# Kernel tuning notes

Hardware: AMD Instinct MI355X
Metric: run time of the kernel (lower is better)

## Reference

```python
import jax, jax.numpy as jnp
import numpy as np

N_NODES = 50000
N_EDGES = 800000
IN_FEAT = 512
HEADS = 4
OUT_FEAT = 64


def setup_inputs() -> dict:
    key = jax.random.key(0)
    k1, k2, k3 = jax.random.split(key, 3)
    x = jax.random.normal(k1, (N_NODES, IN_FEAT), dtype=jnp.float32)
    # W corresponds to nn.Linear(in, heads*out, bias=False).weight: (H*F, in)
    W = jax.random.normal(k2, (HEADS * OUT_FEAT, IN_FEAT), dtype=jnp.float32) * (1.0 / np.sqrt(IN_FEAT))
    edge_index = jax.random.randint(k3, (2, N_EDGES), 0, N_NODES, dtype=jnp.int32)
    return {"x": x, "W": W, "edge_index": edge_index}


def reference(x, W, edge_index):
    # h = W(x) viewed as (N, H, F)
    n = x.shape[0]
    hf = W.shape[0]
    h = (x @ W.T).reshape(n, HEADS, hf // HEADS)
    src, dst = edge_index[0], edge_index[1]
    # scatter-mean of h[src] into dst buckets (single O(E) pass, replaces per-node loop)
    msg = h[src]                                             # (E, H, F)
    summed = jax.ops.segment_sum(msg, dst, num_segments=n)   # (N, H, F)
    cnt = jax.ops.segment_sum(jnp.ones((edge_index.shape[1],), h.dtype), dst, num_segments=n)
    mean = summed / jnp.maximum(cnt, 1.0)[:, None, None]
    # nodes with no in-edges keep their own transformed features
    out = jnp.where((cnt > 0)[:, None, None], mean, h)
    return out.reshape(n, hf)
```

## Files before the change

kernel.cpp:

```cpp
#include <hip/hip_runtime.h>
#include <hip/hip_bf16.h>

#define N_NODES 50000
#define N_EDGES 800000
#define IN_FEAT 512
#define HF 256
#define BM 128
#define BN 256
#define BK 32
#define CAP 64
#define GEMM_BLOCKS 391
#define FILL_BLOCKS 218

typedef short short8 __attribute__((ext_vector_type(8)));
typedef float f32x4 __attribute__((ext_vector_type(4)));

__device__ __forceinline__ unsigned short f2bf(float f) {
    union { float f; unsigned u; } c{f};
    unsigned r = c.u + 0x7FFFu + ((c.u >> 16) & 1u);
    return (unsigned short)(r >> 16);
}
__device__ __forceinline__ float bf2f(unsigned short b) {
    union { unsigned u; float f; } c;
    c.u = ((unsigned)b) << 16;
    return c.f;
}
__device__ __forceinline__ short8 pack8(const float4& a, const float4& b) {
    short8 v;
    v[0] = (short)f2bf(a.x); v[1] = (short)f2bf(a.y);
    v[2] = (short)f2bf(a.z); v[3] = (short)f2bf(a.w);
    v[4] = (short)f2bf(b.x); v[5] = (short)f2bf(b.y);
    v[6] = (short)f2bf(b.z); v[7] = (short)f2bf(b.w);
    return v;
}
__device__ __forceinline__ void gload16(const void* g, void* l) {
    __builtin_amdgcn_global_load_lds(
        (const __attribute__((address_space(1))) unsigned int*)g,
        (__attribute__((address_space(3))) unsigned int*)l, 16, 0, 0);
}

__global__ __launch_bounds__(64) void convw_kernel(const float* __restrict__ Wm,
                                                   unsigned short* __restrict__ Wb) {
    const int row = blockIdx.x;
    const int t = threadIdx.x;
    const int slice = t >> 2;
    const int p = t & 3;
    const int lc = p ^ ((row >> 1) & 3);
    const float* g = Wm + (size_t)row * IN_FEAT + slice * 32 + lc * 8;
    const float4 v0 = *(const float4*)(g);
    const float4 v1 = *(const float4*)(g + 4);
    *(short8*)(Wb + (size_t)row * IN_FEAT + slice * 32 + p * 8) = pack8(v0, v1);
}

__global__ __launch_bounds__(512) void gemm_fill_kernel(const float* __restrict__ X,
                                                        const unsigned short* __restrict__ Wb,
                                                        unsigned short* __restrict__ H,
                                                        const int* __restrict__ ei,
                                                        int* __restrict__ cnt,
                                                        int* __restrict__ bucket) {
    if (blockIdx.x >= GEMM_BLOCKS) {
        const int cb = blockIdx.x - GEMM_BLOCKS;
        const int stride = FILL_BLOCKS * 512;
        for (int e = cb * 512 + threadIdx.x; e < N_EDGES; e += stride) {
            const int src = ei[e];
            const int dst = ei[N_EDGES + e];
            const int pos = atomicAdd(&cnt[dst], 1);
            if (pos < CAP) bucket[dst * CAP + pos] = src;
        }
        return;
    }

    __shared__ float Af[2][BM * BK];
    __shared__ unsigned short Bsh[2][BN * BK];

    const int t    = threadIdx.x;
    const int lane = t & 63;
    const int w    = t >> 6;
    const int wr   = w >> 2;
    const int wc   = w & 3;
    const int brow = blockIdx.x * BM;
    const int l15  = lane & 15;

    const int sa0 = w * 2, sa1 = w * 2 + 1;

    int aro0 = sa0 * 8 + (lane >> 3);
    int aro1 = sa1 * 8 + (lane >> 3);
    int ag0 = brow + aro0; if (ag0 >= N_NODES) ag0 = N_NODES - 1;
    int ag1 = brow + aro1; if (ag1 >= N_NODES) ag1 = N_NODES - 1;
    const int alc0 = ((lane & 7) ^ (aro0 & 7)) * 4;
    const int alc1 = ((lane & 7) ^ (aro1 & 7)) * 4;
    const float* asrc0 = X + (size_t)ag0 * IN_FEAT + alc0;
    const float* asrc1 = X + (size_t)ag1 * IN_FEAT + alc1;

    const int bro0 = sa0 * 16 + (lane >> 2);
    const int bro1 = sa1 * 16 + (lane >> 2);
    const unsigned short* bsrc0 = Wb + (size_t)bro0 * IN_FEAT + (lane & 3) * 8;
    const unsigned short* bsrc1 = Wb + (size_t)bro1 * IN_FEAT + (lane & 3) * 8;

    f32x4 acc[4][4] = {};

    gload16(asrc0, &Af[0][sa0 * 256]);
    gload16(asrc1, &Af[0][sa1 * 256]);
    gload16(bsrc0, &Bsh[0][sa0 * 512]);
    gload16(bsrc1, &Bsh[0][sa1 * 512]);
    __syncthreads();

    int cur = 0;
    for (int kt = 0; kt < IN_FEAT; kt += BK) {
        const int kn = kt + BK;
        if (kn < IN_FEAT) {
            const int nb = cur ^ 1;
            gload16(asrc0 + kn, &Af[nb][sa0 * 256]);
            gload16(asrc1 + kn, &Af[nb][sa1 * 256]);
            gload16(bsrc0 + kn, &Bsh[nb][sa0 * 512]);
            gload16(bsrc1 + kn, &Bsh[nb][sa1 * 512]);
        }

        const int c0 = (lane >> 4) * 2;
        const int cb0 = lane >> 4;
        short8 a[4], b[4];
#pragma unroll
        for (int n = 0; n < 4; ++n) {
            const int rt = wc * 64 + n * 16 + l15;
            b[n] = *(const short8*)(&Bsh[cur][rt * BK + ((cb0 ^ ((rt >> 1) & 3)) << 3)]);
        }
#pragma unroll
        for (int m = 0; m < 4; ++m) {
            const int rt = wr * 64 + m * 16 + l15;
            const float4 x0 = *(const float4*)(&Af[cur][rt * BK + ((c0 ^ (rt & 7)) << 2)]);
            const float4 x1 = *(const float4*)(&Af[cur][rt * BK + (((c0 + 1) ^ (rt & 7)) << 2)]);
            a[m] = pack8(x0, x1);
        }
#pragma unroll
        for (int m = 0; m < 4; ++m)
#pragma unroll
            for (int n = 0; n < 4; ++n)
                acc[m][n] = __builtin_amdgcn_mfma_f32_16x16x32_bf16(a[m], b[n], acc[m][n], 0, 0, 0);

        __syncthreads();
        cur ^= 1;
    }

#pragma unroll
    for (int m = 0; m < 4; ++m) {
        const int row0 = brow + wr * 64 + m * 16 + (lane >> 4) * 4;
#pragma unroll
        for (int n = 0; n < 4; ++n) {
            const int col = wc * 64 + n * 16 + l15;
#pragma unroll
            for (int j = 0; j < 4; ++j) {
                const int row = row0 + j;
                if (row < N_NODES) H[(size_t)row * HF + col] = f2bf(acc[m][n][j]);
            }
        }
    }
}

__global__ __launch_bounds__(256) void aggregate_kernel(const unsigned short* __restrict__ h,
                                                        const int* __restrict__ cnt,
                                                        const int* __restrict__ bucket,
                                                        float* __restrict__ out) {
    const int node = (int)(((size_t)blockIdx.x * blockDim.x + threadIdx.x) >> 6);
    const int lane = threadIdx.x & 63;
    if (node >= N_NODES) return;
    int c = cnt[node];
    if (c > CAP) c = CAP;
    const int base = node * CAP;

    float a0 = 0.f, a1 = 0.f, a2 = 0.f, a3 = 0.f;

    int i = 0;
    for (; i + 4 <= c; i += 4) {
        const int s0 = bucket[base + i + 0];
        const int s1 = bucket[base + i + 1];
        const int s2 = bucket[base + i + 2];
        const int s3 = bucket[base + i + 3];
        const ushort4 v0 = *(const ushort4*)(h + (size_t)s0 * HF + lane * 4);
        const ushort4 v1 = *(const ushort4*)(h + (size_t)s1 * HF + lane * 4);
        const ushort4 v2 = *(const ushort4*)(h + (size_t)s2 * HF + lane * 4);
        const ushort4 v3 = *(const ushort4*)(h + (size_t)s3 * HF + lane * 4);
        a0 += bf2f(v0.x) + bf2f(v1.x) + bf2f(v2.x) + bf2f(v3.x);
        a1 += bf2f(v0.y) + bf2f(v1.y) + bf2f(v2.y) + bf2f(v3.y);
        a2 += bf2f(v0.z) + bf2f(v1.z) + bf2f(v2.z) + bf2f(v3.z);
        a3 += bf2f(v0.w) + bf2f(v1.w) + bf2f(v2.w) + bf2f(v3.w);
    }
    for (; i < c; ++i) {
        const int s0 = bucket[base + i];
        const ushort4 v0 = *(const ushort4*)(h + (size_t)s0 * HF + lane * 4);
        a0 += bf2f(v0.x); a1 += bf2f(v0.y); a2 += bf2f(v0.z); a3 += bf2f(v0.w);
    }

    float4 r;
    if (c > 0) {
        const float inv = 1.0f / (float)c;
        r.x = a0 * inv; r.y = a1 * inv; r.z = a2 * inv; r.w = a3 * inv;
    } else {
        const ushort4 v = *(const ushort4*)(h + (size_t)node * HF + lane * 4);
        r.x = bf2f(v.x); r.y = bf2f(v.y); r.z = bf2f(v.z); r.w = bf2f(v.w);
    }
    *(float4*)(out + (size_t)node * HF + lane * 4) = r;
}

extern "C" void kernel_launch(void* const* d_in, const int* in_sizes, int n_in,
                              void* d_out, int out_size, void* d_ws, size_t ws_size,
                              hipStream_t stream) {
    const float* x = (const float*)d_in[0];
    const float* W = (const float*)d_in[1];
    const int* ei  = (const int*)d_in[2];
    float* out = (float*)d_out;

    char* ws = (char*)d_ws;
    unsigned short* h = (unsigned short*)ws;
    int* bucket = (int*)(ws + (size_t)N_NODES * HF * 2);
    int* cnt    = (int*)((char*)bucket + (size_t)N_NODES * CAP * 4);
    unsigned short* Wb = (unsigned short*)((char*)cnt + (size_t)(N_NODES + 64) * 4);

    hipMemsetAsync(cnt, 0, (size_t)N_NODES * sizeof(int), stream);

    convw_kernel<<<HF, 64, 0, stream>>>(W, Wb);

    gemm_fill_kernel<<<GEMM_BLOCKS + FILL_BLOCKS, 512, 0, stream>>>(x, Wb, h, ei, cnt, bucket);

    aggregate_kernel<<<(N_NODES * 64 + 255) / 256, 256, 0, stream>>>(h, cnt, bucket, out);
}
```

Before: 116.3 us.

## Triple-buffer A tiles, load B directly to registers, fuse counter zeroing

The GEMM now keeps the converted weight operand out of shared memory. Each wave loads its B fragments straight from global memory into registers, one K-step ahead. The X tile uses a three-stage LDS ring with explicit vmcnt waits and a single barrier per iteration instead of two syncthreads, and the final K-step is peeled out of the loop. The separate memset of the edge counters is folded into the weight-conversion kernel to save a launch. The weight swizzle is removed, and in exchange B traffic now goes through per-wave global loads that rely on L2 reuse across blocks.

After: 139.4 us. +19.8%, slower.

```diff
diff --git a/kernel.cpp b/kernel.cpp
--- a/kernel.cpp
+++ b/kernel.cpp
@@ -8,9 +8,12 @@
 #define BM 128
 #define BN 256
 #define BK 32
+#define NT 16
 #define CAP 64
 #define GEMM_BLOCKS 391
 #define FILL_BLOCKS 218
+#define CONV_BLOCKS 256
+#define ZERO_BLOCKS 200
 
 typedef short short8 __attribute__((ext_vector_type(8)));
 typedef float f32x4 __attribute__((ext_vector_type(4)));
@@ -39,17 +42,25 @@
         (__attribute__((address_space(3))) unsigned int*)l, 16, 0, 0);
 }
 
-__global__ __launch_bounds__(64) void convw_kernel(const float* __restrict__ Wm,
-                                                   unsigned short* __restrict__ Wb) {
-    const int row = blockIdx.x;
-    const int t = threadIdx.x;
-    const int slice = t >> 2;
-    const int p = t & 3;
-    const int lc = p ^ ((row >> 1) & 3);
-    const float* g = Wm + (size_t)row * IN_FEAT + slice * 32 + lc * 8;
-    const float4 v0 = *(const float4*)(g);
-    const float4 v1 = *(const float4*)(g + 4);
-    *(short8*)(Wb + (size_t)row * IN_FEAT + slice * 32 + p * 8) = pack8(v0, v1);
+__global__ __launch_bounds__(64) void convw_init_kernel(const float* __restrict__ Wm,
+                                                        unsigned short* __restrict__ Wb,
+                                                        int* __restrict__ cnt) {
+    if (blockIdx.x < CONV_BLOCKS) {
+        const int row = blockIdx.x;
+        const int t = threadIdx.x;
+        const float* g = Wm + (size_t)row * IN_FEAT + t * 8;
+        const float4 v0 = *(const float4*)(g);
+        const float4 v1 = *(const float4*)(g + 4);
+        *(short8*)(Wb + (size_t)row * IN_FEAT + t * 8) = pack8(v0, v1);
+    } else {
+        const int i = ((blockIdx.x - CONV_BLOCKS) * 64 + threadIdx.x) * 4;
+        if (i + 3 < N_NODES) {
+            int4 z = {0, 0, 0, 0};
+            *(int4*)(cnt + i) = z;
+        } else {
+            for (int k = 0; k < 4 && i + k < N_NODES; ++k) cnt[i + k] = 0;
+        }
+    }
 }
 
 __global__ __launch_bounds__(512) void gemm_fill_kernel(const float* __restrict__ X,
@@ -70,8 +81,7 @@
         return;
     }
 
-    __shared__ float Af[2][BM * BK];
-    __shared__ unsigned short Bsh[2][BN * BK];
+    __shared__ float Af[3][BM * BK];
 
     const int t    = threadIdx.x;
     const int lane = t & 63;
@@ -82,63 +92,86 @@
     const int l15  = lane & 15;
 
     const int sa0 = w * 2, sa1 = w * 2 + 1;
-
-    int aro0 = sa0 * 8 + (lane >> 3);
-    int aro1 = sa1 * 8 + (lane >> 3);
+    const int aro0 = sa0 * 8 + (lane >> 3);
+    const int aro1 = sa1 * 8 + (lane >> 3);
     int ag0 = brow + aro0; if (ag0 >= N_NODES) ag0 = N_NODES - 1;
     int ag1 = brow + aro1; if (ag1 >= N_NODES) ag1 = N_NODES - 1;
-    const int alc0 = ((lane & 7) ^ (aro0 & 7)) * 4;
-    const int alc1 = ((lane & 7) ^ (aro1 & 7)) * 4;
-    const float* asrc0 = X + (size_t)ag0 * IN_FEAT + alc0;
-    const float* asrc1 = X + (size_t)ag1 * IN_FEAT + alc1;
-
-    const int bro0 = sa0 * 16 + (lane >> 2);
-    const int bro1 = sa1 * 16 + (lane >> 2);
-    const unsigned short* bsrc0 = Wb + (size_t)bro0 * IN_FEAT + (lane & 3) * 8;
-    const unsigned short* bsrc1 = Wb + (size_t)bro1 * IN_FEAT + (lane & 3) * 8;
+    const float* asrc0 = X + (size_t)ag0 * IN_FEAT + ((lane & 7) ^ (aro0 & 7)) * 4;
+    const float* asrc1 = X + (size_t)ag1 * IN_FEAT + ((lane & 7) ^ (aro1 & 7)) * 4;
+
+    const unsigned short* bp[4];
+#pragma unroll
+    for (int n = 0; n < 4; ++n)
+        bp[n] = Wb + (size_t)(wc * 64 + n * 16 + l15) * IN_FEAT + (lane >> 4) * 8;
 
     f32x4 acc[4][4] = {};
+    short8 bcur[4], bnext[4];
 
     gload16(asrc0, &Af[0][sa0 * 256]);
     gload16(asrc1, &Af[0][sa1 * 256]);
-    gload16(bsrc0, &Bsh[0][sa0 * 512]);
-    gload16(bsrc1, &Bsh[0][sa1 * 512]);
-    __syncthreads();
-
-    int cur = 0;
-    for (int kt = 0; kt < IN_FEAT; kt += BK) {
-        const int kn = kt + BK;
-        if (kn < IN_FEAT) {
-            const int nb = cur ^ 1;
+    gload16(asrc0 + BK, &Af[1][sa0 * 256]);
+    gload16(asrc1 + BK, &Af[1][sa1 * 256]);
+    __builtin_amdgcn_sched_barrier(0);
+#pragma unroll
+    for (int n = 0; n < 4; ++n) bcur[n] = *(const short8*)(bp[n]);
+
+    const int c0 = (lane >> 4) * 2;
+
+    for (int tt = 0; tt < NT - 1; ++tt) {
+        asm volatile("s_waitcnt vmcnt(6)" ::: "memory");
+        __builtin_amdgcn_sched_barrier(0);
+        __builtin_amdgcn_s_barrier();
+        __builtin_amdgcn_sched_barrier(0);
+
+        if (tt + 2 < NT) {
+            const int kn = (tt + 2) * BK;
+            const int nb = (tt + 2) % 3;
             gload16(asrc0 + kn, &Af[nb][sa0 * 256]);
             gload16(asrc1 + kn, &Af[nb][sa1 * 256]);
-            gload16(bsrc0 + kn, &Bsh[nb][sa0 * 512]);
-            gload16(bsrc1 + kn, &Bsh[nb][sa1 * 512]);
-        }
-
-        const int c0 = (lane >> 4) * 2;
-        const int cb0 = lane >> 4;
-        short8 a[4], b[4];
-#pragma unroll
-        for (int n = 0; n < 4; ++n) {
-            const int rt = wc * 64 + n * 16 + l15;
-            b[n] = *(const short8*)(&Bsh[cur][rt * BK + ((cb0 ^ ((rt >> 1) & 3)) << 3)]);
-        }
+        }
+        __builtin_amdgcn_sched_barrier(0);
+
+        const int kb = (tt + 1) * BK;
+#pragma unroll
+        for (int n = 0; n < 4; ++n) bnext[n] = *(const short8*)(bp[n] + kb);
+
+        const int cur = tt % 3;
+        short8 a[4];
 #pragma unroll
         for (int m = 0; m < 4; ++m) {
             const int rt = wr * 64 + m * 16 + l15;
-            const float4 x0 = *(const float4*)(&Af[cur][rt * BK + ((c0 ^ (rt & 7)) << 2)]);
-            const float4 x1 = *(const float4*)(&Af[cur][rt * BK + (((c0 + 1) ^ (rt & 7)) << 2)]);
+            const float4 x0 = *(const float4*)(&Af[cur][rt * 32 + ((c0 ^ (rt & 7)) << 2)]);
+            const float4 x1 = *(const float4*)(&Af[cur][rt * 32 + (((c0 + 1) ^ (rt & 7)) << 2)]);
             a[m] = pack8(x0, x1);
         }
 #pragma unroll
         for (int m = 0; m < 4; ++m)
 #pragma unroll
             for (int n = 0; n < 4; ++n)
-                acc[m][n] = __builtin_amdgcn_mfma_f32_16x16x32_bf16(a[m], b[n], acc[m][n], 0, 0, 0);
-
-        __syncthreads();
-        cur ^= 1;
+                acc[m][n] = __builtin_amdgcn_mfma_f32_16x16x32_bf16(a[m], bcur[n], acc[m][n], 0, 0, 0);
+#pragma unroll
+        for (int n = 0; n < 4; ++n) bcur[n] = bnext[n];
+    }
+
+    asm volatile("s_waitcnt vmcnt(0)" ::: "memory");
+    __builtin_amdgcn_sched_barrier(0);
+    __builtin_amdgcn_s_barrier();
+    __builtin_amdgcn_sched_barrier(0);
+    {
+        const int cur = (NT - 1) % 3;
+        short8 a[4];
+#pragma unroll
+        for (int m = 0; m < 4; ++m) {
+            const int rt = wr * 64 + m * 16 + l15;
+            const float4 x0 = *(const float4*)(&Af[cur][rt * 32 + ((c0 ^ (rt & 7)) << 2)]);
+            const float4 x1 = *(const float4*)(&Af[cur][rt * 32 + (((c0 + 1) ^ (rt & 7)) << 2)]);
+            a[m] = pack8(x0, x1);
+        }
+#pragma unroll
+        for (int m = 0; m < 4; ++m)
+#pragma unroll
+            for (int n = 0; n < 4; ++n)
+                acc[m][n] = __builtin_amdgcn_mfma_f32_16x16x32_bf16(a[m], bcur[n], acc[m][n], 0, 0, 0);
     }
 
 #pragma unroll
@@ -215,9 +248,7 @@
     int* cnt    = (int*)((char*)bucket + (size_t)N_NODES * CAP * 4);
     unsigned short* Wb = (unsigned short*)((char*)cnt + (size_t)(N_NODES + 64) * 4);
 
-    hipMemsetAsync(cnt, 0, (size_t)N_NODES * sizeof(int), stream);
-
-    convw_kernel<<<HF, 64, 0, stream>>>(W, Wb);
+    convw_init_kernel<<<CONV_BLOCKS + ZERO_BLOCKS, 64, 0, stream>>>(W, Wb, cnt);
 
     gemm_fill_kernel<<<GEMM_BLOCKS + FILL_BLOCKS, 512, 0, stream>>>(x, Wb, h, ei, cnt, bucket);
 
```
